# Performance work log

Measured on AMD Instinct MI355X. Metric: run time of the kernel, lower is better.

Reference implementation:

```python
import jax, jax.numpy as jnp
import numpy as np

B, S, HID, H, DB = 4, 2048, 512, 8, 8
DH = HID // H  # head dim = 64


def setup_inputs() -> dict:
    key = jax.random.key(0)
    ks = jax.random.split(key, 14)
    s = 0.02
    return {
        "q": jax.random.normal(ks[0], (B, S, HID), jnp.float32),
        "k": jax.random.normal(ks[1], (B, S, HID), jnp.float32),
        "v": jax.random.normal(ks[2], (B, S, HID), jnp.float32),
        "attn_bias": jax.random.normal(ks[3], (B, S, S, DB), jnp.float32),
        "Wq": jax.random.normal(ks[4], (HID, HID), jnp.float32) * s,
        "bq": jnp.zeros((HID,), jnp.float32),
        "Wk": jax.random.normal(ks[5], (HID, HID), jnp.float32) * s,
        "bk": jnp.zeros((HID,), jnp.float32),
        "Wv": jax.random.normal(ks[6], (HID, HID), jnp.float32) * s,
        "bv": jnp.zeros((HID,), jnp.float32),
        "Wb": jax.random.normal(ks[7], (H, DB), jnp.float32) * s,
        "bb": jnp.zeros((H,), jnp.float32),
        "Wo": jax.random.normal(ks[8], (HID, HID), jnp.float32) * s,
        "bo": jnp.zeros((HID,), jnp.float32),
    }


def reference(q, k, v, attn_bias, Wq, bq, Wk, bk, Wv, bv, Wb, bb, Wo, bo):
    scale = DH ** (-0.5)
    # projections: torch Linear is x @ W.T + b
    qh = (q @ Wq.T + bq).reshape(B, S, H, DH).transpose(0, 2, 1, 3)  # [B,H,S,D]
    kh = (k @ Wk.T + bk).reshape(B, S, H, DH).transpose(0, 2, 1, 3)
    vh = (v @ Wv.T + bv).reshape(B, S, H, DH).transpose(0, 2, 1, 3)
    scores = jnp.einsum("bhqd,bhkd->bhqk", qh * scale, kh)  # [B,H,S,S]
    bias = (attn_bias @ Wb.T + bb).transpose(0, 3, 1, 2)  # [B,H,S,S]
    attn = jax.nn.softmax(scores + bias, axis=-1)
    out = jnp.einsum("bhqk,bhkd->bhqd", attn, vh)  # [B,H,S,D]
    out = out.transpose(0, 2, 1, 3).reshape(B, S, HID)
    return out @ Wo.T + bo
```

## Files before the change

kernel.cpp:

```cpp
#include <hip/hip_runtime.h>
#include <cstdint>
#include <cstddef>

#define BB 4
#define SS 2048
#define HIDD 512
#define HH 8
#define DHH 64
#define DBB 8

typedef __attribute__((ext_vector_type(4))) float f32x4;
typedef __attribute__((ext_vector_type(8))) short s16x8;
typedef __attribute__((ext_vector_type(4))) short s16x4;

__device__ __forceinline__ short f2bf(float x) {
  unsigned u = __builtin_bit_cast(unsigned, x);
  u += 0x7FFFu + ((u >> 16) & 1u);
  return (short)(u >> 16);
}
__device__ __forceinline__ float bf2f(short s) {
  unsigned u = ((unsigned)(unsigned short)s) << 16;
  return __builtin_bit_cast(float, u);
}

template <int MODE>
__global__ __launch_bounds__(256) void gemm_xwT(const float* __restrict__ X,
                                                const float* __restrict__ W,
                                                const float* __restrict__ bias,
                                                float* __restrict__ outF,
                                                short* __restrict__ outB) {
  __shared__ short xs[64][40];
  __shared__ short wsh[64][40];
  const int tid = threadIdx.x;
  const int wave = tid >> 6, lane = tid & 63;
  const int quad = lane >> 4, m16 = lane & 15;
  const int m0 = blockIdx.x * 64, n0 = blockIdx.y * 64;
  const int wm = (wave & 1) * 32, wn = (wave >> 1) * 32;

  f32x4 acc[2][2];
#pragma unroll
  for (int a = 0; a < 2; a++)
#pragma unroll
    for (int b2 = 0; b2 < 2; b2++) acc[a][b2] = (f32x4){0.f, 0.f, 0.f, 0.f};

  for (int k0 = 0; k0 < HIDD; k0 += 32) {
#pragma unroll
    for (int i = 0; i < 2; i++) {
      int c = tid + i * 256;
      int row = c >> 3, kc = c & 7;
      f32x4 xv = *(const f32x4*)(X + (size_t)(m0 + row) * HIDD + k0 + kc * 4);
      f32x4 wv = *(const f32x4*)(W + (size_t)(n0 + row) * HIDD + k0 + kc * 4);
      s16x4 xb, wb2;
#pragma unroll
      for (int j = 0; j < 4; j++) { xb[j] = f2bf(xv[j]); wb2[j] = f2bf(wv[j]); }
      *(s16x4*)(&xs[row][kc * 4]) = xb;
      *(s16x4*)(&wsh[row][kc * 4]) = wb2;
    }
    __syncthreads();
    s16x8 af[2], bfr[2];
    af[0] = *(const s16x8*)(&xs[wm + m16][quad * 8]);
    af[1] = *(const s16x8*)(&xs[wm + 16 + m16][quad * 8]);
    bfr[0] = *(const s16x8*)(&wsh[wn + m16][quad * 8]);
    bfr[1] = *(const s16x8*)(&wsh[wn + 16 + m16][quad * 8]);
    acc[0][0] = __builtin_amdgcn_mfma_f32_16x16x32_bf16(af[0], bfr[0], acc[0][0], 0, 0, 0);
    acc[0][1] = __builtin_amdgcn_mfma_f32_16x16x32_bf16(af[0], bfr[1], acc[0][1], 0, 0, 0);
    acc[1][0] = __builtin_amdgcn_mfma_f32_16x16x32_bf16(af[1], bfr[0], acc[1][0], 0, 0, 0);
    acc[1][1] = __builtin_amdgcn_mfma_f32_16x16x32_bf16(af[1], bfr[1], acc[1][1], 0, 0, 0);
    __syncthreads();
  }

#pragma unroll
  for (int a = 0; a < 2; a++)
#pragma unroll
    for (int b2 = 0; b2 < 2; b2++)
#pragma unroll
      for (int r = 0; r < 4; r++) {
        int m = m0 + wm + a * 16 + quad * 4 + r;
        int n = n0 + wn + b2 * 16 + m16;
        float val = acc[a][b2][r] + bias[n];
        if (MODE == 0) {
          int b_ = m >> 11, s = m & 2047, h = n >> 6, d = n & 63;
          outB[((size_t)(b_ * HH + h) * SS + s) * DHH + d] = f2bf(val * 0.125f);
        } else if (MODE == 1) {
          int b_ = m >> 11, s = m & 2047, h = n >> 6, d = n & 63;
          outB[((size_t)(b_ * HH + h) * SS + s) * DHH + d] = f2bf(val);
        } else if (MODE == 2) {
          int b_ = m >> 11, s = m & 2047, h = n >> 6, d = n & 63;
          outB[((size_t)(b_ * HH + h) * DHH + d) * SS + s] = f2bf(val);
        } else {
          outF[(size_t)m * HIDD + n] = val;
        }
      }
}

__global__ __launch_bounds__(512, 8) void flash_attn(const short* __restrict__ qh,
                                                     const short* __restrict__ kh,
                                                     const short* __restrict__ vh,
                                                     const float* __restrict__ attn_bias,
                                                     const float* __restrict__ Wb,
                                                     const float* __restrict__ bb,
                                                     float* __restrict__ attn_out) {
  __shared__ short bp[2][HH][16][34];
  __shared__ short pbuf[HH][16][40];

  const int tid = threadIdx.x;
  const int wave = tid >> 6, lane = tid & 63;
  const int quad = lane >> 4, m16 = lane & 15;
  const int wg = (int)blockIdx.x;
  const int lb = ((wg & 7) << 6) | (wg >> 3);
  const int b = lb >> 7;
  const int q0 = (lb & 127) << 4;
  const int h = wave;

  const size_t qoff = ((size_t)((b * HH + h) * SS) + q0 + m16) * DHH;
  s16x8 qf0 = *(const s16x8*)(qh + qoff + quad * 8);
  s16x8 qf1 = *(const s16x8*)(qh + qoff + 32 + quad * 8);

  const short* kbase = kh + ((size_t)(b * HH + h) * SS + m16) * DHH + quad * 8;
  const short* vbase = vh + ((size_t)((b * HH + h) * DHH) + m16) * SS + quad * 8;

  const int ql = tid >> 5, kl = tid & 31;
  const float* bptr = attn_bias + ((size_t)(b * SS + q0 + ql) * SS + kl) * DBB;

  f32x4 oacc[4];
#pragma unroll
  for (int dt = 0; dt < 4; dt++) oacc[dt] = (f32x4){0.f, 0.f, 0.f, 0.f};
  float m_r[4], l_r[4];
#pragma unroll
  for (int r = 0; r < 4; r++) { m_r[r] = -3.0e38f; l_r[r] = 0.f; }

  {
    f32x4 c0 = *(const f32x4*)(bptr);
    f32x4 c1 = *(const f32x4*)(bptr + 4);
#pragma unroll
    for (int h2 = 0; h2 < 8; h2++) {
      float a2 = bb[h2];
#pragma unroll
      for (int d = 0; d < 4; d++) {
        a2 += c0[d] * Wb[h2 * 8 + d];
        a2 += c1[d] * Wb[h2 * 8 + 4 + d];
      }
      bp[0][h2][ql][kl] = f2bf(a2);
    }
  }
  __syncthreads();

  for (int it = 0; it < 64; ++it) {
    const int k0 = it << 5;
    const int cur = it & 1;

    f32x4 n0, n1;
    if (it < 63) {
      const float* np = bptr + (size_t)(k0 + 32) * DBB;
      n0 = *(const f32x4*)(np);
      n1 = *(const f32x4*)(np + 4);
    }

    f32x4 sc[2];
#pragma unroll
    for (int nt = 0; nt < 2; nt++) {
      const short* kp = kbase + (size_t)(k0 + nt * 16) * DHH;
      s16x8 kf0 = *(const s16x8*)(kp);
      s16x8 kf1 = *(const s16x8*)(kp + 32);
      f32x4 z = (f32x4){0.f, 0.f, 0.f, 0.f};
      z = __builtin_amdgcn_mfma_f32_16x16x32_bf16(qf0, kf0, z, 0, 0, 0);
      z = __builtin_amdgcn_mfma_f32_16x16x32_bf16(qf1, kf1, z, 0, 0, 0);
      sc[nt] = z;
    }

#pragma unroll
    for (int r = 0; r < 4; r++) {
      int row = quad * 4 + r;
      float s0 = sc[0][r] + bf2f(bp[cur][h][row][m16]);
      float s1 = sc[1][r] + bf2f(bp[cur][h][row][16 + m16]);
      float v = fmaxf(s0, s1);
      v = fmaxf(v, __shfl_xor(v, 1, 16));
      v = fmaxf(v, __shfl_xor(v, 2, 16));
      v = fmaxf(v, __shfl_xor(v, 4, 16));
      v = fmaxf(v, __shfl_xor(v, 8, 16));
      float nm = fmaxf(m_r[r], v);
      float al = __expf(m_r[r] - nm);
      m_r[r] = nm;
      float p0 = __expf(s0 - nm);
      float p1 = __expf(s1 - nm);
      float rs = p0 + p1;
      rs += __shfl_xor(rs, 1, 16);
      rs += __shfl_xor(rs, 2, 16);
      rs += __shfl_xor(rs, 4, 16);
      rs += __shfl_xor(rs, 8, 16);
      l_r[r] = l_r[r] * al + rs;
#pragma unroll
      for (int dt = 0; dt < 4; dt++) oacc[dt][r] *= al;
      pbuf[wave][row][m16] = f2bf(p0);
      pbuf[wave][row][16 + m16] = f2bf(p1);
    }

    s16x8 pf = *(const s16x8*)(&pbuf[wave][m16][quad * 8]);
#pragma unroll
    for (int dt = 0; dt < 4; dt++) {
      const short* vp = vbase + (size_t)(dt * 16) * SS + k0;
      s16x8 vf = *(const s16x8*)(vp);
      oacc[dt] = __builtin_amdgcn_mfma_f32_16x16x32_bf16(pf, vf, oacc[dt], 0, 0, 0);
    }

    if (it < 63) {
#pragma unroll
      for (int h2 = 0; h2 < 8; h2++) {
        float a2 = bb[h2];
#pragma unroll
        for (int d = 0; d < 4; d++) {
          a2 += n0[d] * Wb[h2 * 8 + d];
          a2 += n1[d] * Wb[h2 * 8 + 4 + d];
        }
        bp[cur ^ 1][h2][ql][kl] = f2bf(a2);
      }
    }
    __syncthreads();
  }

#pragma unroll
  for (int dt = 0; dt < 4; dt++)
#pragma unroll
    for (int r = 0; r < 4; r++) {
      float val = oacc[dt][r] / l_r[r];
      attn_out[(size_t)(b * SS + q0 + quad * 4 + r) * HIDD + h * 64 + dt * 16 + m16] = val;
    }
}

extern "C" void kernel_launch(void* const* d_in, const int* in_sizes, int n_in,
                              void* d_out, int out_size, void* d_ws, size_t ws_size,
                              hipStream_t stream) {
  const float* q = (const float*)d_in[0];
  const float* k = (const float*)d_in[1];
  const float* v = (const float*)d_in[2];
  const float* attn_bias = (const float*)d_in[3];
  const float* Wq = (const float*)d_in[4];
  const float* bq = (const float*)d_in[5];
  const float* Wk = (const float*)d_in[6];
  const float* bk = (const float*)d_in[7];
  const float* Wv = (const float*)d_in[8];
  const float* bv = (const float*)d_in[9];
  const float* Wb = (const float*)d_in[10];
  const float* bb = (const float*)d_in[11];
  const float* Wo = (const float*)d_in[12];
  const float* bo = (const float*)d_in[13];
  float* out = (float*)d_out;

  short* qh = (short*)d_ws;
  short* kh = qh + (size_t)4194304;
  short* vh = kh + (size_t)4194304;
  float* attn_ws = (float*)(vh + (size_t)4194304);

  dim3 g(128, 8), blk(256);
  gemm_xwT<0><<<g, blk, 0, stream>>>(q, Wq, bq, nullptr, qh);
  gemm_xwT<1><<<g, blk, 0, stream>>>(k, Wk, bk, nullptr, kh);
  gemm_xwT<2><<<g, blk, 0, stream>>>(v, Wv, bv, nullptr, vh);
  flash_attn<<<512, 512, 0, stream>>>(qh, kh, vh, attn_bias, Wb, bb, attn_ws);
  gemm_xwT<3><<<g, blk, 0, stream>>>(attn_ws, Wo, bo, out, nullptr);
}
```

Baseline: 1.216 ms.

## Pre-convert activations and weights to bf16 and use register-tiled 128x128 GEMMs

Adds conversion kernels that cast the fp32 inputs and the four weight matrices to bf16 once. The projection GEMMs now read bf16 fragments straight from global memory with no LDS staging, using 128x128 tiles with 4x4 MFMA tiles per wave and a swizzled block order. The attention kernel writes its output as bf16 so the output projection reads half the bytes, and its launch-bounds occupancy hint drops from 8 to 4. The aim is to cut redundant fp32 loads and conversions and the LDS round trips, at the cost of extra kernel launches and an intermediate bf16 buffer.

```diff
diff --git a/kernel.cpp b/kernel.cpp
--- a/kernel.cpp
+++ b/kernel.cpp
@@ -11,7 +11,6 @@
 
 typedef __attribute__((ext_vector_type(4))) float f32x4;
 typedef __attribute__((ext_vector_type(8))) short s16x8;
-typedef __attribute__((ext_vector_type(4))) short s16x4;
 
 __device__ __forceinline__ short f2bf(float x) {
   unsigned u = __builtin_bit_cast(unsigned, x);
@@ -23,61 +22,81 @@
   return __builtin_bit_cast(float, u);
 }
 
+__global__ __launch_bounds__(256) void cvt_f32_bf16(const float* __restrict__ src,
+                                                    short* __restrict__ dst, int n8) {
+  int i = blockIdx.x * 256 + threadIdx.x;
+  if (i < n8) {
+    f32x4 a = *(const f32x4*)(src + (size_t)i * 8);
+    f32x4 b = *(const f32x4*)(src + (size_t)i * 8 + 4);
+    s16x8 o;
+#pragma unroll
+    for (int j = 0; j < 4; j++) { o[j] = f2bf(a[j]); o[4 + j] = f2bf(b[j]); }
+    *(s16x8*)(dst + (size_t)i * 8) = o;
+  }
+}
+
+__global__ __launch_bounds__(256) void cvt_w4(const float* __restrict__ w0, const float* __restrict__ w1,
+                                              const float* __restrict__ w2, const float* __restrict__ w3,
+                                              short* __restrict__ dst) {
+  const float* s = (blockIdx.y == 0) ? w0 : (blockIdx.y == 1) ? w1 : (blockIdx.y == 2) ? w2 : w3;
+  short* d = dst + (size_t)blockIdx.y * 262144;
+  int i = blockIdx.x * 256 + threadIdx.x;
+  f32x4 a = *(const f32x4*)(s + (size_t)i * 8);
+  f32x4 b = *(const f32x4*)(s + (size_t)i * 8 + 4);
+  s16x8 o;
+#pragma unroll
+  for (int j = 0; j < 4; j++) { o[j] = f2bf(a[j]); o[4 + j] = f2bf(b[j]); }
+  *(s16x8*)(d + (size_t)i * 8) = o;
+}
+
 template <int MODE>
-__global__ __launch_bounds__(256) void gemm_xwT(const float* __restrict__ X,
-                                                const float* __restrict__ W,
-                                                const float* __restrict__ bias,
-                                                float* __restrict__ outF,
-                                                short* __restrict__ outB) {
-  __shared__ short xs[64][40];
-  __shared__ short wsh[64][40];
+__global__ __launch_bounds__(256) void gemm_bf16(const short* __restrict__ A,
+                                                 const short* __restrict__ W,
+                                                 const float* __restrict__ bias,
+                                                 float* __restrict__ outF,
+                                                 short* __restrict__ outB) {
   const int tid = threadIdx.x;
   const int wave = tid >> 6, lane = tid & 63;
   const int quad = lane >> 4, m16 = lane & 15;
-  const int m0 = blockIdx.x * 64, n0 = blockIdx.y * 64;
-  const int wm = (wave & 1) * 32, wn = (wave >> 1) * 32;
-
-  f32x4 acc[2][2];
-#pragma unroll
-  for (int a = 0; a < 2; a++)
-#pragma unroll
-    for (int b2 = 0; b2 < 2; b2++) acc[a][b2] = (f32x4){0.f, 0.f, 0.f, 0.f};
+  const int wg = (int)blockIdx.x;
+  const int j6 = wg & 63;
+  const int mt = ((j6 & 7) << 3) | (j6 >> 3);
+  const int nt = wg >> 6;
+  const int m0 = mt << 7, n0 = nt << 7;
+  const int wm = (wave & 1) << 6, wn = (wave >> 1) << 6;
+
+  f32x4 acc[4][4];
+#pragma unroll
+  for (int i = 0; i < 4; i++)
+#pragma unroll
+    for (int j = 0; j < 4; j++) acc[i][j] = (f32x4){0.f, 0.f, 0.f, 0.f};
+
+  const short* Ab = A + (size_t)(m0 + wm + m16) * HIDD + quad * 8;
+  const short* Wp = W + (size_t)(n0 + wn + m16) * HIDD + quad * 8;
 
   for (int k0 = 0; k0 < HIDD; k0 += 32) {
-#pragma unroll
-    for (int i = 0; i < 2; i++) {
-      int c = tid + i * 256;
-      int row = c >> 3, kc = c & 7;
-      f32x4 xv = *(const f32x4*)(X + (size_t)(m0 + row) * HIDD + k0 + kc * 4);
-      f32x4 wv = *(const f32x4*)(W + (size_t)(n0 + row) * HIDD + k0 + kc * 4);
-      s16x4 xb, wb2;
-#pragma unroll
-      for (int j = 0; j < 4; j++) { xb[j] = f2bf(xv[j]); wb2[j] = f2bf(wv[j]); }
-      *(s16x4*)(&xs[row][kc * 4]) = xb;
-      *(s16x4*)(&wsh[row][kc * 4]) = wb2;
-    }
-    __syncthreads();
-    s16x8 af[2], bfr[2];
-    af[0] = *(const s16x8*)(&xs[wm + m16][quad * 8]);
-    af[1] = *(const s16x8*)(&xs[wm + 16 + m16][quad * 8]);
-    bfr[0] = *(const s16x8*)(&wsh[wn + m16][quad * 8]);
-    bfr[1] = *(const s16x8*)(&wsh[wn + 16 + m16][quad * 8]);
-    acc[0][0] = __builtin_amdgcn_mfma_f32_16x16x32_bf16(af[0], bfr[0], acc[0][0], 0, 0, 0);
-    acc[0][1] = __builtin_amdgcn_mfma_f32_16x16x32_bf16(af[0], bfr[1], acc[0][1], 0, 0, 0);
-    acc[1][0] = __builtin_amdgcn_mfma_f32_16x16x32_bf16(af[1], bfr[0], acc[1][0], 0, 0, 0);
-    acc[1][1] = __builtin_amdgcn_mfma_f32_16x16x32_bf16(af[1], bfr[1], acc[1][1], 0, 0, 0);
-    __syncthreads();
-  }
-
-#pragma unroll
-  for (int a = 0; a < 2; a++)
-#pragma unroll
-    for (int b2 = 0; b2 < 2; b2++)
+    s16x8 af[4], bfr[4];
+#pragma unroll
+    for (int i = 0; i < 4; i++) {
+      af[i] = *(const s16x8*)(Ab + (size_t)(i * 16) * HIDD + k0);
+      bfr[i] = *(const s16x8*)(Wp + (size_t)(i * 16) * HIDD + k0);
+    }
+#pragma unroll
+    for (int i = 0; i < 4; i++)
+#pragma unroll
+      for (int j = 0; j < 4; j++)
+        acc[i][j] = __builtin_amdgcn_mfma_f32_16x16x32_bf16(af[i], bfr[j], acc[i][j], 0, 0, 0);
+  }
+
+#pragma unroll
+  for (int i = 0; i < 4; i++)
+#pragma unroll
+    for (int j = 0; j < 4; j++)
 #pragma unroll
       for (int r = 0; r < 4; r++) {
-        int m = m0 + wm + a * 16 + quad * 4 + r;
-        int n = n0 + wn + b2 * 16 + m16;
-        float val = acc[a][b2][r] + bias[n];
+        int m = m0 + wm + i * 16 + quad * 4 + r;
+        int n = n0 + wn + j * 16 + m16;
+        float val = acc[i][j][r] + bias[n];
         if (MODE == 0) {
           int b_ = m >> 11, s = m & 2047, h = n >> 6, d = n & 63;
           outB[((size_t)(b_ * HH + h) * SS + s) * DHH + d] = f2bf(val * 0.125f);
@@ -93,13 +112,13 @@
       }
 }
 
-__global__ __launch_bounds__(512, 8) void flash_attn(const short* __restrict__ qh,
+__global__ __launch_bounds__(512, 4) void flash_attn(const short* __restrict__ qh,
                                                      const short* __restrict__ kh,
                                                      const short* __restrict__ vh,
                                                      const float* __restrict__ attn_bias,
                                                      const float* __restrict__ Wb,
                                                      const float* __restrict__ bb,
-                                                     float* __restrict__ attn_out) {
+                                                     short* __restrict__ attn_out) {
   __shared__ short bp[2][HH][16][34];
   __shared__ short pbuf[HH][16][40];
 
@@ -158,14 +177,14 @@
 
     f32x4 sc[2];
 #pragma unroll
-    for (int nt = 0; nt < 2; nt++) {
-      const short* kp = kbase + (size_t)(k0 + nt * 16) * DHH;
+    for (int nt2 = 0; nt2 < 2; nt2++) {
+      const short* kp = kbase + (size_t)(k0 + nt2 * 16) * DHH;
       s16x8 kf0 = *(const s16x8*)(kp);
       s16x8 kf1 = *(const s16x8*)(kp + 32);
       f32x4 z = (f32x4){0.f, 0.f, 0.f, 0.f};
       z = __builtin_amdgcn_mfma_f32_16x16x32_bf16(qf0, kf0, z, 0, 0, 0);
       z = __builtin_amdgcn_mfma_f32_16x16x32_bf16(qf1, kf1, z, 0, 0, 0);
-      sc[nt] = z;
+      sc[nt2] = z;
     }
 
 #pragma unroll
@@ -223,7 +242,7 @@
 #pragma unroll
     for (int r = 0; r < 4; r++) {
       float val = oacc[dt][r] / l_r[r];
-      attn_out[(size_t)(b * SS + q0 + quad * 4 + r) * HIDD + h * 64 + dt * 16 + m16] = val;
+      attn_out[(size_t)(b * SS + q0 + quad * 4 + r) * HIDD + h * 64 + dt * 16 + m16] = f2bf(val);
     }
 }
 
@@ -249,12 +268,16 @@
   short* qh = (short*)d_ws;
   short* kh = qh + (size_t)4194304;
   short* vh = kh + (size_t)4194304;
-  float* attn_ws = (float*)(vh + (size_t)4194304);
-
-  dim3 g(128, 8), blk(256);
-  gemm_xwT<0><<<g, blk, 0, stream>>>(q, Wq, bq, nullptr, qh);
-  gemm_xwT<1><<<g, blk, 0, stream>>>(k, Wk, bk, nullptr, kh);
-  gemm_xwT<2><<<g, blk, 0, stream>>>(v, Wv, bv, nullptr, vh);
-  flash_attn<<<512, 512, 0, stream>>>(qh, kh, vh, attn_bias, Wb, bb, attn_ws);
-  gemm_xwT<3><<<g, blk, 0, stream>>>(attn_ws, Wo, bo, out, nullptr);
-}
+  short* S = vh + (size_t)4194304;
+  short* W4 = S + (size_t)4194304;
+
+  cvt_w4<<<dim3(128, 4), 256, 0, stream>>>(Wq, Wk, Wv, Wo, W4);
+  cvt_f32_bf16<<<2048, 256, 0, stream>>>(q, S, 524288);
+  gemm_bf16<0><<<256, 256, 0, stream>>>(S, W4, bq, nullptr, qh);
+  cvt_f32_bf16<<<2048, 256, 0, stream>>>(k, S, 524288);
+  gemm_bf16<1><<<256, 256, 0, stream>>>(S, W4 + 262144, bk, nullptr, kh);
+  cvt_f32_bf16<<<2048, 256, 0, stream>>>(v, S, 524288);
+  gemm_bf16<2><<<256, 256, 0, stream>>>(S, W4 + 524288, bv, nullptr, vh);
+  flash_attn<<<512, 512, 0, stream>>>(qh, kh, vh, attn_bias, Wb, bb, S);
+  gemm_bf16<3><<<256, 256, 0, stream>>>(S, W4 + 786432, bo, out, nullptr);
+}
```

Result: faster. 1.041 ms (-14.3%).
